# Performance work log

Hardware: AMD Instinct MI355X
Metric: run time of the kernel (lower is better)

The kernel has to match this reference:

```python
import jax, jax.numpy as jnp
import numpy as np

C = 256          # in_channels
CI = 128         # inter_channels = C // reduction
N_B, H, W = 4, 64, 64


def setup_inputs() -> dict:
    key = jax.random.key(0)
    ks = jax.random.split(key, 9)
    std = 0.01
    inp = {
        "x": jax.random.normal(ks[0], (N_B, C, H, W), dtype=jnp.float32),
        # 1x1 conv weights stored as [out_ch, in_ch]
        "w_g": jax.random.normal(ks[1], (CI, C), dtype=jnp.float32) * std,
        "b_g": jnp.zeros((CI,), dtype=jnp.float32),
        "w_theta": jax.random.normal(ks[2], (CI, C), dtype=jnp.float32) * std,
        "b_theta": jnp.zeros((CI,), dtype=jnp.float32),
        "w_phi": jax.random.normal(ks[3], (CI, C), dtype=jnp.float32) * std,
        "b_phi": jnp.zeros((CI,), dtype=jnp.float32),
        # conv_out: use small random instead of exact zeros so output is non-trivial
        "w_out": jax.random.normal(ks[4], (C, CI), dtype=jnp.float32) * std,
        "b_out": jnp.zeros((C,), dtype=jnp.float32),
    }
    return inp


def reference(x, w_g, b_g, w_theta, b_theta, w_phi, b_phi, w_out, b_out):
    n, c, h, w = x.shape
    nhw = h * w
    xf = x.reshape(n, c, nhw)                                   # [n, C, N]
    # 1x1 convs == channel matmuls
    g_x = jnp.einsum('ncs,oc->nso', xf, w_g) + b_g              # [n, N, CI]
    theta_x = jnp.einsum('ncs,oc->nso', xf, w_theta) + b_theta  # [n, N, CI]
    phi_x = jnp.einsum('ncs,oc->nos', xf, w_phi) + b_phi[None, :, None]  # [n, CI, N]
    # pairwise weights: [n, N, N]
    pw = jnp.einsum('nqc,ncs->nqs', theta_x, phi_x)
    # faithful to original: DIVIDE by d**-0.5 (i.e. multiply by sqrt(d))
    pw = pw / (theta_x.shape[-1] ** (-0.5))
    pw = jax.nn.softmax(pw, axis=-1)
    y = jnp.einsum('nqs,nsc->nqc', pw, g_x)                     # [n, N, CI]
    y = y.transpose(0, 2, 1).reshape(n, -1, h, w)               # [n, CI, H, W]
    out = jnp.einsum('nchw,oc->nohw', y, w_out) + b_out[None, :, None, None]
    return x + out
```

## Files before the change

### kernel.cpp

```cpp
#include <hip/hip_runtime.h>
#include <cmath>

typedef __attribute__((ext_vector_type(8))) short bf16x8;
typedef __attribute__((ext_vector_type(4))) float f32x4;
typedef __attribute__((ext_vector_type(16))) float f32x16;

#define MFMA16(a,b,c)  __builtin_amdgcn_mfma_f32_16x16x32_bf16((a),(b),(c),0,0,0)
#define MFMA32(a,b,c)  __builtin_amdgcn_mfma_f32_32x32x16_bf16((a),(b),(c),0,0,0)

#if __has_builtin(__builtin_amdgcn_exp2f)
#define EXP2F(x) __builtin_amdgcn_exp2f(x)
#else
#define EXP2F(x) exp2f(x)
#endif

#define KSCALE 16.3222312f

#define NB 4
#define CH 256
#define CI 128
#define NS 4096

__device__ __forceinline__ unsigned short f2bf(float f) {
    unsigned int u = __builtin_bit_cast(unsigned int, f);
    u += 0x7fffu + ((u >> 16) & 1u);
    return (unsigned short)(u >> 16);
}
__device__ __forceinline__ unsigned int pk2(float lo, float hi) {
    return (unsigned int)f2bf(lo) | ((unsigned int)f2bf(hi) << 16);
}
__device__ __forceinline__ unsigned int pkt(float lo, float hi) {
    return __builtin_amdgcn_perm(__builtin_bit_cast(unsigned int, hi),
                                 __builtin_bit_cast(unsigned int, lo), 0x07060302u);
}
__device__ __forceinline__ float bf2f(unsigned int ush) {
    return __builtin_bit_cast(float, ush << 16);
}

__device__ __forceinline__ void plswap(unsigned int& wLow, unsigned int& wHigh) {
    asm volatile("v_permlane32_swap_b32 %0, %1" : "+v"(wLow), "+v"(wHigh));
}

__device__ __forceinline__ f32x16 zero16() {
    f32x16 v;
#pragma unroll
    for (int i = 0; i < 16; i++) v[i] = 0.f;
    return v;
}

__device__ __forceinline__ void gload16(void* lds, const void* g) {
    __builtin_amdgcn_global_load_lds(
        (const __attribute__((address_space(1))) unsigned int*)g,
        (__attribute__((address_space(3))) unsigned int*)lds,
        16, 0, 0);
}

__global__ void wcvt_kernel(const float* __restrict__ w_g, const float* __restrict__ w_th,
                            const float* __restrict__ w_ph, const float* __restrict__ w_out,
                            const float* __restrict__ b_g, const float* __restrict__ b_th,
                            const float* __restrict__ b_ph,
                            unsigned short* __restrict__ wbf, float* __restrict__ bsc) {
    int i = blockIdx.x * 256 + threadIdx.x;
    float v;
    if (i < 32768)        v = w_g[i];
    else if (i < 65536)   v = w_th[i - 32768] * KSCALE;
    else if (i < 98304)   v = w_ph[i - 65536];
    else                  v = w_out[i - 98304];
    wbf[i] = f2bf(v);
    if (i < 128)          bsc[i] = b_g[i];
    else if (i < 256)     bsc[i] = b_th[i - 128] * KSCALE;
    else if (i < 384)     bsc[i] = b_ph[i - 256];
}

__global__ __launch_bounds__(512, 2)
void proj_kernel(const float* __restrict__ x,
                 const unsigned short* __restrict__ wbf, const float* __restrict__ bsc,
                 unsigned short* __restrict__ theta,
                 unsigned short* __restrict__ phi,
                 unsigned short* __restrict__ gT) {
    const int tid  = threadIdx.x;
    const int wid  = tid >> 6;
    const int lane = tid & 63;
    const int quad = lane >> 4;
    const int l15  = lane & 15;
    const int stile = blockIdx.x;
    const int n     = blockIdx.y;
    const int s0    = stile * 64;

    const float* xN = x + (size_t)n * CH * NS;

    __shared__ unsigned int xp[64 * 128];

#pragma unroll
    for (int i = 0; i < 4; i++) {
        int t  = i * 512 + tid;
        int s4 = t & 15;
        int cp = t >> 4;
        const float* p0 = xN + (size_t)(2 * cp) * NS + s0 + s4 * 4;
        float4 a = *(const float4*)p0;
        float4 b = *(const float4*)(p0 + NS);
        int col = (((cp >> 2) ^ (s4 & 7)) << 2) | (cp & 3);
        unsigned int* xr = xp + (s4 * 4) * 128 + col;
        xr[0]   = pk2(a.x, b.x);
        xr[128] = pk2(a.y, b.y);
        xr[256] = pk2(a.z, b.z);
        xr[384] = pk2(a.w, b.w);
    }
    __syncthreads();

    const int srow = (wid & 3) * 16 + l15;
    const int oh   = wid >> 2;
    const int sw7  = (srow >> 2) & 7;
#pragma unroll
    for (int wi = 0; wi < 3; wi++) {
        f32x4 acc[4];
#pragma unroll
        for (int ot = 0; ot < 4; ot++) acc[ot] = (f32x4){0.f, 0.f, 0.f, 0.f};
        const unsigned short* W = wbf + (size_t)wi * 32768 + (size_t)oh * 64 * CH;
#pragma unroll
        for (int kc = 0; kc < 8; kc++) {
            bf16x8 af = *(const bf16x8*)(&xp[srow * 128 + (((kc * 4 + quad) ^ sw7) << 2)]);
#pragma unroll
            for (int ot = 0; ot < 4; ot++) {
                bf16x8 wf = *(const bf16x8*)(W + (size_t)(ot * 16 + l15) * CH + kc * 32 + quad * 8);
                acc[ot] = MFMA16(af, wf, acc[ot]);
            }
        }
        const float* Bv = bsc + wi * 128 + oh * 64;
#pragma unroll
        for (int ot = 0; ot < 4; ot++) {
            int o = oh * 64 + ot * 16 + l15;
            float bias = Bv[ot * 16 + l15];
#pragma unroll
            for (int r = 0; r < 4; r++) {
                int sg = s0 + (wid & 3) * 16 + quad * 4 + r;
                float v = acc[ot][r] + bias;
                if (wi == 0)
                    gT[((size_t)n * CI + o) * NS + sg] = f2bf(v);
                else if (wi == 1)
                    theta[((size_t)n * NS + sg) * CI + o] = f2bf(v);
                else
                    phi[((size_t)n * NS + sg) * CI + o] = f2bf(v);
            }
        }
    }
}

__global__ __launch_bounds__(256, 2)
void attn_kernel(const unsigned short* __restrict__ theta,
                 const unsigned short* __restrict__ phi,
                 const unsigned short* __restrict__ gT,
                 unsigned short* __restrict__ Opart,
                 float* __restrict__ lbuf) {
    const int tid  = threadIdx.x;
    const int wid  = tid >> 6;
    const int lane = tid & 63;
    const int l31  = lane & 31;
    const int lh32 = lane >> 5;
    const int sn    = blockIdx.x;
    const int split = sn >> 2;
    const int n     = sn & 3;
    const int qb    = blockIdx.y;
    const int qbase = qb * 128 + wid * 32;

    const unsigned short* thN = theta + (size_t)n * NS * CI;
    const unsigned short* phN = phi   + (size_t)n * NS * CI;
    const unsigned short* gN  = gT    + (size_t)n * CI * NS;

    __shared__ unsigned short smem[32768];
    unsigned short* Kb = smem;
    unsigned short* Vb = smem + 16384;

    bf16x8 qf[8];
#pragma unroll
    for (int kc = 0; kc < 8; kc++)
        qf[kc] = *(const bf16x8*)(thN + (size_t)(qbase + l31) * CI + kc * 16 + lh32 * 8);

    f32x16 O[4];
#pragma unroll
    for (int ct = 0; ct < 4; ct++) O[ct] = zero16();
    float lrun = 0.f;

    const int sbase0 = split * 1024;
    const int lh16 = lane >> 4, lm16 = lane & 15;
    const int lh8  = lane >> 3, lm8  = lane & 7;

#pragma unroll
    for (int i = 0; i < 4; i++) {
        int seg = wid * 4 + i;
        int s   = seg * 4 + lh16;
        int j   = lm16 ^ (s & 15);
        gload16(Kb + seg * 512, phN + (size_t)(sbase0 + s) * CI + j * 8);
    }
#pragma unroll
    for (int i = 0; i < 4; i++) {
        int seg = wid * 4 + i;
        int c   = seg * 8 + lh8;
        int j   = lm8 ^ (c & 7);
        gload16(Vb + seg * 512, gN + (size_t)c * NS + sbase0 + j * 8);
    }

    for (int ck = 0; ck < 16; ck++) {
        const int cur = ck & 1, nxt = cur ^ 1;
        unsigned short* Kc = Kb + cur * 8192;
        unsigned short* Vc = Vb + cur * 8192;
        __syncthreads();

        if (ck + 1 < 16) {
            const int sb1 = sbase0 + (ck + 1) * 64;
#pragma unroll
            for (int i = 0; i < 4; i++) {
                int seg = wid * 4 + i;
                int s   = seg * 4 + lh16;
                int j   = lm16 ^ (s & 15);
                gload16(Kb + nxt * 8192 + seg * 512, phN + (size_t)(sb1 + s) * CI + j * 8);
            }
#pragma unroll
            for (int i = 0; i < 4; i++) {
                int seg = wid * 4 + i;
                int c   = seg * 8 + lh8;
                int j   = lm8 ^ (c & 7);
                gload16(Vb + nxt * 8192 + seg * 512, gN + (size_t)c * NS + sb1 + j * 8);
            }
        }

        f32x16 S[2];
        S[0] = zero16(); S[1] = zero16();
        __builtin_amdgcn_s_setprio(1);
#pragma unroll
        for (int sb = 0; sb < 2; sb++) {
#pragma unroll
            for (int kc = 0; kc < 8; kc++) {
                int s = sb * 32 + l31;
                bf16x8 kf = *(const bf16x8*)(Kc + s * 128 + (((kc * 2 + lh32) ^ (s & 15)) * 8));
                S[sb] = MFMA32(kf, qf[kc], S[sb]);
            }
        }
        __builtin_amdgcn_s_setprio(0);

        bf16x8 pf[4];
        float lsum = 0.f;
#pragma unroll
        for (int ks = 0; ks < 4; ks++) {
            const int sb = ks >> 1, b = ks & 1;
            float pA[4], pB[4];
#pragma unroll
            for (int m = 0; m < 4; m++) {
                pA[m] = EXP2F(S[sb][(2 * b) * 4 + m]);
                pB[m] = EXP2F(S[sb][(2 * b + 1) * 4 + m]);
            }
            lsum += ((pA[0] + pA[1]) + (pA[2] + pA[3]))
                  + ((pB[0] + pB[1]) + (pB[2] + pB[3]));
            unsigned int wA0 = pkt(pA[0], pA[1]);
            unsigned int wA1 = pkt(pA[2], pA[3]);
            unsigned int wB0 = pkt(pB[0], pB[1]);
            unsigned int wB1 = pkt(pB[2], pB[3]);
            plswap(wA0, wB0);
            plswap(wA1, wB1);
            union { unsigned int u[4]; bf16x8 v; } P;
            P.u[0] = wA0; P.u[1] = wA1; P.u[2] = wB0; P.u[3] = wB1;
            pf[ks] = P.v;
        }
        lrun += lsum;

        __builtin_amdgcn_s_setprio(1);
#pragma unroll
        for (int ks = 0; ks < 4; ks++) {
#pragma unroll
            for (int ct = 0; ct < 4; ct++) {
                int c = ct * 32 + l31;
                bf16x8 vf = *(const bf16x8*)(Vc + c * 64 + (((ks * 2 + lh32) ^ (c & 7)) * 8));
                O[ct] = MFMA32(vf, pf[ks], O[ct]);
            }
        }
        __builtin_amdgcn_s_setprio(0);
    }

    __syncthreads();
    float* tb = (float*)smem + wid * 2048;
    const size_t obase = ((size_t)(split * NB + n)) * NS * CI;
#pragma unroll
    for (int pass = 0; pass < 2; pass++) {
#pragma unroll
        for (int cti = 0; cti < 2; cti++) {
            const int ct = pass * 2 + cti;
#pragma unroll
            for (int g = 0; g < 4; g++) {
                const int c_local = cti * 32 + 8 * g + 4 * lh32;
                const int slot = (c_local >> 2) ^ (l31 & 15);
                f32x4 v;
                v[0] = O[ct][4 * g + 0]; v[1] = O[ct][4 * g + 1];
                v[2] = O[ct][4 * g + 2]; v[3] = O[ct][4 * g + 3];
                *(f32x4*)(tb + l31 * 64 + slot * 4) = v;
            }
        }
#pragma unroll
        for (int i = 0; i < 8; i++) {
            const int qr  = i * 4 + (lane >> 4);
            const int lin = lane & 15;
            f32x4 v = *(const f32x4*)(tb + qr * 64 + ((lin ^ (qr & 15)) * 4));
            uint2 w;
            w.x = pk2(v[0], v[1]);
            w.y = pk2(v[2], v[3]);
            *(uint2*)(Opart + obase + (size_t)(qbase + qr) * CI + pass * 64 + lin * 4) = w;
        }
    }
    lrun += __shfl_xor(lrun, 32);
    if (lane < 32)
        lbuf[(split * NB + n) * NS + qbase + l31] = lrun;
}

__global__ __launch_bounds__(256, 4)
void outproj_kernel(const float* __restrict__ x,
                    const unsigned short* __restrict__ wbf,
                    const float* __restrict__ b_out,
                    const unsigned short* __restrict__ Opart,
                    const float* __restrict__ lbuf,
                    float* __restrict__ out) {
    const int tid  = threadIdx.x;
    const int wid  = tid >> 6;
    const int lane = tid & 63;
    const int quad = lane >> 4;
    const int l15  = lane & 15;
    const int oh = blockIdx.y;
    const int n  = blockIdx.z;
    const int sw = blockIdx.x * 64 + wid * 16;
    const int T  = NB * NS;

    const int srow = n * NS + sw + l15;
    float l = 0.f;
#pragma unroll
    for (int k = 0; k < 4; k++) l += lbuf[k * T + srow];
    float rinv = 1.0f / l;

    bf16x8 yb[4];
#pragma unroll
    for (int kc = 0; kc < 4; kc++) {
        float f0 = 0.f, f1 = 0.f, f2 = 0.f, f3 = 0.f;
        float f4 = 0.f, f5 = 0.f, f6 = 0.f, f7 = 0.f;
#pragma unroll
        for (int k = 0; k < 4; k++) {
            uint4 v = *(const uint4*)(Opart + ((size_t)k * T + srow) * CI + kc * 32 + quad * 8);
            f0 += bf2f(v.x & 0xffffu); f1 += bf2f(v.x >> 16);
            f2 += bf2f(v.y & 0xffffu); f3 += bf2f(v.y >> 16);
            f4 += bf2f(v.z & 0xffffu); f5 += bf2f(v.z >> 16);
            f6 += bf2f(v.w & 0xffffu); f7 += bf2f(v.w >> 16);
        }
        union { unsigned int uu[4]; bf16x8 vv; } r;
        r.uu[0] = pk2(f0 * rinv, f1 * rinv);
        r.uu[1] = pk2(f2 * rinv, f3 * rinv);
        r.uu[2] = pk2(f4 * rinv, f5 * rinv);
        r.uu[3] = pk2(f6 * rinv, f7 * rinv);
        yb[kc] = r.vv;
    }

    const unsigned short* wob = wbf + 3 * 32768 + (size_t)oh * 128 * CI;
    f32x4 acc[8];
#pragma unroll
    for (int ot = 0; ot < 8; ot++) acc[ot] = (f32x4){0.f, 0.f, 0.f, 0.f};
#pragma unroll
    for (int kc = 0; kc < 4; kc++) {
#pragma unroll
        for (int ot = 0; ot < 8; ot++) {
            bf16x8 wa = *(const bf16x8*)(wob + (size_t)(ot * 16 + l15) * CI + kc * 32 + quad * 8);
            acc[ot] = MFMA16(wa, yb[kc], acc[ot]);
        }
    }
#pragma unroll
    for (int ot = 0; ot < 8; ot++) {
#pragma unroll
        for (int r = 0; r < 4; r++) {
            int o = oh * 128 + ot * 16 + quad * 4 + r;
            size_t idx = ((size_t)n * CH + o) * NS + sw + l15;
            out[idx] = x[idx] + acc[ot][r] + b_out[o];
        }
    }
}

extern "C" void kernel_launch(void* const* d_in, const int* in_sizes, int n_in,
                              void* d_out, int out_size, void* d_ws, size_t ws_size,
                              hipStream_t stream) {
    const float* x     = (const float*)d_in[0];
    const float* w_g   = (const float*)d_in[1];
    const float* b_g   = (const float*)d_in[2];
    const float* w_th  = (const float*)d_in[3];
    const float* b_th  = (const float*)d_in[4];
    const float* w_ph  = (const float*)d_in[5];
    const float* b_ph  = (const float*)d_in[6];
    const float* w_out = (const float*)d_in[7];
    const float* b_out = (const float*)d_in[8];
    float* out = (float*)d_out;

    char* ws = (char*)d_ws;
    unsigned short* theta = (unsigned short*)(ws + 0);
    unsigned short* phi   = (unsigned short*)(ws + 4194304);
    unsigned short* gT    = (unsigned short*)(ws + 8388608);
    unsigned short* Opart = (unsigned short*)(ws + 12582912);
    float* lbuf  = (float*)(ws + 29360128);
    unsigned short* wbf = (unsigned short*)(ws + 29622272);
    float* bsc   = (float*)(ws + 29884416);

    wcvt_kernel<<<512, 256, 0, stream>>>(w_g, w_th, w_ph, w_out, b_g, b_th, b_ph, wbf, bsc);
    proj_kernel<<<dim3(64, NB), 512, 0, stream>>>(x, wbf, bsc, theta, phi, gT);
    attn_kernel<<<dim3(16, 32), 256, 0, stream>>>(theta, phi, gT, Opart, lbuf);
    outproj_kernel<<<dim3(64, 2, NB), 256, 0, stream>>>(x, wbf, b_out, Opart, lbuf, out);
}
```

Measured before the change: 160.4 us.

## Process two query tiles per wave and double the key split count

Each wave now handles 64 query rows as two 32-row tiles, so every K and V fragment read from LDS feeds two MFMAs instead of one. This halves LDS traffic per unit of math. To keep the grid size, the key dimension is split 8 ways instead of 4, and the outproj kernel now sums 8 partial outputs and row sums. Risks are higher register pressure (doubled O accumulators and Q fragments at launch bounds of 2 blocks per CU), plus twice the partial-output write and read traffic, and a larger workspace.

New measurement: 209.9 us. 1.31x slower.

```diff
diff --git a/kernel.cpp b/kernel.cpp
--- a/kernel.cpp
+++ b/kernel.cpp
@@ -20,6 +20,7 @@
 #define CH 256
 #define CI 128
 #define NS 4096
+#define SPLIT 8
 
 __device__ __forceinline__ unsigned short f2bf(float f) {
     unsigned int u = __builtin_bit_cast(unsigned int, f);
@@ -161,7 +162,7 @@
     const int split = sn >> 2;
     const int n     = sn & 3;
     const int qb    = blockIdx.y;
-    const int qbase = qb * 128 + wid * 32;
+    const int qbase = qb * 256 + wid * 64;
 
     const unsigned short* thN = theta + (size_t)n * NS * CI;
     const unsigned short* phN = phi   + (size_t)n * NS * CI;
@@ -171,17 +172,21 @@
     unsigned short* Kb = smem;
     unsigned short* Vb = smem + 16384;
 
-    bf16x8 qf[8];
-#pragma unroll
-    for (int kc = 0; kc < 8; kc++)
-        qf[kc] = *(const bf16x8*)(thN + (size_t)(qbase + l31) * CI + kc * 16 + lh32 * 8);
-
-    f32x16 O[4];
-#pragma unroll
-    for (int ct = 0; ct < 4; ct++) O[ct] = zero16();
-    float lrun = 0.f;
-
-    const int sbase0 = split * 1024;
+    bf16x8 qf[2][8];
+#pragma unroll
+    for (int qt = 0; qt < 2; qt++)
+#pragma unroll
+        for (int kc = 0; kc < 8; kc++)
+            qf[qt][kc] = *(const bf16x8*)(thN + (size_t)(qbase + qt * 32 + l31) * CI + kc * 16 + lh32 * 8);
+
+    f32x16 O[2][4];
+#pragma unroll
+    for (int qt = 0; qt < 2; qt++)
+#pragma unroll
+        for (int ct = 0; ct < 4; ct++) O[qt][ct] = zero16();
+    float lrun[2] = {0.f, 0.f};
+
+    const int sbase0 = split * 512;
     const int lh16 = lane >> 4, lm16 = lane & 15;
     const int lh8  = lane >> 3, lm8  = lane & 7;
 
@@ -200,13 +205,13 @@
         gload16(Vb + seg * 512, gN + (size_t)c * NS + sbase0 + j * 8);
     }
 
-    for (int ck = 0; ck < 16; ck++) {
+    for (int ck = 0; ck < 8; ck++) {
         const int cur = ck & 1, nxt = cur ^ 1;
         unsigned short* Kc = Kb + cur * 8192;
         unsigned short* Vc = Vb + cur * 8192;
         __syncthreads();
 
-        if (ck + 1 < 16) {
+        if (ck + 1 < 8) {
             const int sb1 = sbase0 + (ck + 1) * 64;
 #pragma unroll
             for (int i = 0; i < 4; i++) {
@@ -224,90 +229,101 @@
             }
         }
 
-        f32x16 S[2];
-        S[0] = zero16(); S[1] = zero16();
-        __builtin_amdgcn_s_setprio(1);
 #pragma unroll
         for (int sb = 0; sb < 2; sb++) {
+            f32x16 S0 = zero16(), S1 = zero16();
+            __builtin_amdgcn_s_setprio(1);
 #pragma unroll
             for (int kc = 0; kc < 8; kc++) {
                 int s = sb * 32 + l31;
                 bf16x8 kf = *(const bf16x8*)(Kc + s * 128 + (((kc * 2 + lh32) ^ (s & 15)) * 8));
-                S[sb] = MFMA32(kf, qf[kc], S[sb]);
-            }
-        }
-        __builtin_amdgcn_s_setprio(0);
-
-        bf16x8 pf[4];
-        float lsum = 0.f;
-#pragma unroll
-        for (int ks = 0; ks < 4; ks++) {
-            const int sb = ks >> 1, b = ks & 1;
-            float pA[4], pB[4];
-#pragma unroll
-            for (int m = 0; m < 4; m++) {
-                pA[m] = EXP2F(S[sb][(2 * b) * 4 + m]);
-                pB[m] = EXP2F(S[sb][(2 * b + 1) * 4 + m]);
-            }
-            lsum += ((pA[0] + pA[1]) + (pA[2] + pA[3]))
-                  + ((pB[0] + pB[1]) + (pB[2] + pB[3]));
-            unsigned int wA0 = pkt(pA[0], pA[1]);
-            unsigned int wA1 = pkt(pA[2], pA[3]);
-            unsigned int wB0 = pkt(pB[0], pB[1]);
-            unsigned int wB1 = pkt(pB[2], pB[3]);
-            plswap(wA0, wB0);
-            plswap(wA1, wB1);
-            union { unsigned int u[4]; bf16x8 v; } P;
-            P.u[0] = wA0; P.u[1] = wA1; P.u[2] = wB0; P.u[3] = wB1;
-            pf[ks] = P.v;
-        }
-        lrun += lsum;
-
-        __builtin_amdgcn_s_setprio(1);
-#pragma unroll
-        for (int ks = 0; ks < 4; ks++) {
-#pragma unroll
-            for (int ct = 0; ct < 4; ct++) {
-                int c = ct * 32 + l31;
-                bf16x8 vf = *(const bf16x8*)(Vc + c * 64 + (((ks * 2 + lh32) ^ (c & 7)) * 8));
-                O[ct] = MFMA32(vf, pf[ks], O[ct]);
-            }
-        }
-        __builtin_amdgcn_s_setprio(0);
+                S0 = MFMA32(kf, qf[0][kc], S0);
+                S1 = MFMA32(kf, qf[1][kc], S1);
+            }
+            __builtin_amdgcn_s_setprio(0);
+
+            bf16x8 pf[2][2];
+#pragma unroll
+            for (int qt = 0; qt < 2; qt++) {
+                const f32x16& S = qt ? S1 : S0;
+                float lsum = 0.f;
+#pragma unroll
+                for (int b = 0; b < 2; b++) {
+                    float pA[4], pB[4];
+#pragma unroll
+                    for (int m = 0; m < 4; m++) {
+                        pA[m] = EXP2F(S[(2 * b) * 4 + m]);
+                        pB[m] = EXP2F(S[(2 * b + 1) * 4 + m]);
+                    }
+                    lsum += ((pA[0] + pA[1]) + (pA[2] + pA[3]))
+                          + ((pB[0] + pB[1]) + (pB[2] + pB[3]));
+                    unsigned int wA0 = pkt(pA[0], pA[1]);
+                    unsigned int wA1 = pkt(pA[2], pA[3]);
+                    unsigned int wB0 = pkt(pB[0], pB[1]);
+                    unsigned int wB1 = pkt(pB[2], pB[3]);
+                    plswap(wA0, wB0);
+                    plswap(wA1, wB1);
+                    union { unsigned int u[4]; bf16x8 v; } P;
+                    P.u[0] = wA0; P.u[1] = wA1; P.u[2] = wB0; P.u[3] = wB1;
+                    pf[qt][b] = P.v;
+                }
+                lrun[qt] += lsum;
+            }
+
+            __builtin_amdgcn_s_setprio(1);
+#pragma unroll
+            for (int b = 0; b < 2; b++) {
+                const int ks = sb * 2 + b;
+#pragma unroll
+                for (int ct = 0; ct < 4; ct++) {
+                    int c = ct * 32 + l31;
+                    bf16x8 vf = *(const bf16x8*)(Vc + c * 64 + (((ks * 2 + lh32) ^ (c & 7)) * 8));
+                    O[0][ct] = MFMA32(vf, pf[0][b], O[0][ct]);
+                    O[1][ct] = MFMA32(vf, pf[1][b], O[1][ct]);
+                }
+            }
+            __builtin_amdgcn_s_setprio(0);
+        }
     }
 
     __syncthreads();
     float* tb = (float*)smem + wid * 2048;
     const size_t obase = ((size_t)(split * NB + n)) * NS * CI;
 #pragma unroll
-    for (int pass = 0; pass < 2; pass++) {
-#pragma unroll
-        for (int cti = 0; cti < 2; cti++) {
-            const int ct = pass * 2 + cti;
-#pragma unroll
-            for (int g = 0; g < 4; g++) {
-                const int c_local = cti * 32 + 8 * g + 4 * lh32;
-                const int slot = (c_local >> 2) ^ (l31 & 15);
-                f32x4 v;
-                v[0] = O[ct][4 * g + 0]; v[1] = O[ct][4 * g + 1];
-                v[2] = O[ct][4 * g + 2]; v[3] = O[ct][4 * g + 3];
-                *(f32x4*)(tb + l31 * 64 + slot * 4) = v;
-            }
-        }
-#pragma unroll
-        for (int i = 0; i < 8; i++) {
-            const int qr  = i * 4 + (lane >> 4);
-            const int lin = lane & 15;
-            f32x4 v = *(const f32x4*)(tb + qr * 64 + ((lin ^ (qr & 15)) * 4));
-            uint2 w;
-            w.x = pk2(v[0], v[1]);
-            w.y = pk2(v[2], v[3]);
-            *(uint2*)(Opart + obase + (size_t)(qbase + qr) * CI + pass * 64 + lin * 4) = w;
-        }
-    }
-    lrun += __shfl_xor(lrun, 32);
-    if (lane < 32)
-        lbuf[(split * NB + n) * NS + qbase + l31] = lrun;
+    for (int qt = 0; qt < 2; qt++) {
+#pragma unroll
+        for (int pass = 0; pass < 2; pass++) {
+#pragma unroll
+            for (int cti = 0; cti < 2; cti++) {
+                const int ct = pass * 2 + cti;
+#pragma unroll
+                for (int g = 0; g < 4; g++) {
+                    const int c_local = cti * 32 + 8 * g + 4 * lh32;
+                    const int slot = (c_local >> 2) ^ (l31 & 15);
+                    f32x4 v;
+                    v[0] = O[qt][ct][4 * g + 0]; v[1] = O[qt][ct][4 * g + 1];
+                    v[2] = O[qt][ct][4 * g + 2]; v[3] = O[qt][ct][4 * g + 3];
+                    *(f32x4*)(tb + l31 * 64 + slot * 4) = v;
+                }
+            }
+#pragma unroll
+            for (int i = 0; i < 8; i++) {
+                const int qr  = i * 4 + (lane >> 4);
+                const int lin = lane & 15;
+                f32x4 v = *(const f32x4*)(tb + qr * 64 + ((lin ^ (qr & 15)) * 4));
+                uint2 w;
+                w.x = pk2(v[0], v[1]);
+                w.y = pk2(v[2], v[3]);
+                *(uint2*)(Opart + obase + (size_t)(qbase + qt * 32 + qr) * CI + pass * 64 + lin * 4) = w;
+            }
+        }
+    }
+    lrun[0] += __shfl_xor(lrun[0], 32);
+    lrun[1] += __shfl_xor(lrun[1], 32);
+    if (lane < 32) {
+        lbuf[(split * NB + n) * NS + qbase + l31]      = lrun[0];
+        lbuf[(split * NB + n) * NS + qbase + 32 + l31] = lrun[1];
+    }
 }
 
 __global__ __launch_bounds__(256, 4)
@@ -330,7 +346,7 @@
     const int srow = n * NS + sw + l15;
     float l = 0.f;
 #pragma unroll
-    for (int k = 0; k < 4; k++) l += lbuf[k * T + srow];
+    for (int k = 0; k < SPLIT; k++) l += lbuf[k * T + srow];
     float rinv = 1.0f / l;
 
     bf16x8 yb[4];
@@ -339,7 +355,7 @@
         float f0 = 0.f, f1 = 0.f, f2 = 0.f, f3 = 0.f;
         float f4 = 0.f, f5 = 0.f, f6 = 0.f, f7 = 0.f;
 #pragma unroll
-        for (int k = 0; k < 4; k++) {
+        for (int k = 0; k < SPLIT; k++) {
             uint4 v = *(const uint4*)(Opart + ((size_t)k * T + srow) * CI + kc * 32 + quad * 8);
             f0 += bf2f(v.x & 0xffffu); f1 += bf2f(v.x >> 16);
             f2 += bf2f(v.y & 0xffffu); f3 += bf2f(v.y >> 16);
@@ -396,12 +412,12 @@
     unsigned short* phi   = (unsigned short*)(ws + 4194304);
     unsigned short* gT    = (unsigned short*)(ws + 8388608);
     unsigned short* Opart = (unsigned short*)(ws + 12582912);
-    float* lbuf  = (float*)(ws + 29360128);
-    unsigned short* wbf = (unsigned short*)(ws + 29622272);
-    float* bsc   = (float*)(ws + 29884416);
+    float* lbuf  = (float*)(ws + 46137344);
+    unsigned short* wbf = (unsigned short*)(ws + 46661632);
+    float* bsc   = (float*)(ws + 46923776);
 
     wcvt_kernel<<<512, 256, 0, stream>>>(w_g, w_th, w_ph, w_out, b_g, b_th, b_ph, wbf, bsc);
     proj_kernel<<<dim3(64, NB), 512, 0, stream>>>(x, wbf, bsc, theta, phi, gT);
-    attn_kernel<<<dim3(16, 32), 256, 0, stream>>>(theta, phi, gT, Opart, lbuf);
+    attn_kernel<<<dim3(32, 16), 256, 0, stream>>>(theta, phi, gT, Opart, lbuf);
     outproj_kernel<<<dim3(64, 2, NB), 256, 0, stream>>>(x, wbf, b_out, Opart, lbuf, out);
 }
```
